# Performance work log

Hardware: AMD Instinct MI355X
Metric: run time of the kernel (lower is better)

The kernel has to match this reference:

```python
import jax, jax.numpy as jnp
import numpy as np

jax.config.update("jax_enable_x64", True)  # original casts scores to float64

D_MODEL = 1024
NUM_HEADS = 16
DEPTH = D_MODEL // NUM_HEADS
B = 2
SQK = 1025  # q/k seq len; scores sliced [1:, :-1] -> 1024
SV = 1024   # v / mask seq len


def _split_heads(x, batch):
    # (B, S, D) -> (B, H, S, depth)
    s = x.shape[1]
    return x.reshape(batch, s, NUM_HEADS, DEPTH).transpose(0, 2, 1, 3)


def setup_inputs() -> dict:
    key = jax.random.key(0)
    ks = jax.random.split(key, 12)
    sc = 1.0 / np.sqrt(D_MODEL)
    inp = {
        "v": jax.random.normal(ks[0], (B, SV, D_MODEL), dtype=jnp.float32),
        "k": jax.random.normal(ks[1], (B, SQK, D_MODEL), dtype=jnp.float32),
        "q": jax.random.normal(ks[2], (B, SQK, D_MODEL), dtype=jnp.float32),
        "mask": jax.random.randint(ks[3], (B, SV, SV), 0, 2, dtype=jnp.int32),
        "Wq0": jax.random.normal(ks[4], (D_MODEL, D_MODEL), dtype=jnp.float32) * sc,
        "bq0": jnp.zeros((D_MODEL,), dtype=jnp.float32),
        "Wk0": jax.random.normal(ks[5], (D_MODEL, D_MODEL), dtype=jnp.float32) * sc,
        "bk0": jnp.zeros((D_MODEL,), dtype=jnp.float32),
        "Wv": jax.random.normal(ks[6], (D_MODEL, D_MODEL), dtype=jnp.float32) * sc,
        "bv": jnp.zeros((D_MODEL,), dtype=jnp.float32),
        "Wo": jax.random.normal(ks[7], (D_MODEL, D_MODEL), dtype=jnp.float32) * sc,
        "bo": jnp.zeros((D_MODEL,), dtype=jnp.float32),
    }
    return inp


def reference(v, k, q, mask, Wq0, bq0, Wk0, bk0, Wv, bv, Wo, bo):
    batch = q.shape[0]
    # projections (wq/wk of the original layer are unused in call)
    qq = q @ Wq0 + bq0                      # (B, SQK, D)
    kk = k @ Wk0 + bk0                      # (B, SQK, D)
    vv = v @ Wv + bv                        # (B, SV, D)
    qh = _split_heads(qq, batch)            # (B, H, SQK, depth)
    kh = _split_heads(kk, batch)
    vh = _split_heads(vv, batch)            # (B, H, SV, depth)

    # custom attention: matmul -> slice -> relu/scale -> fp64 -> mask -> softmax
    scores = jnp.einsum("bhqd,bhkd->bhqk", qh, kh)          # (B,H,SQK,SQK)
    scores = scores[:, :, 1:, :-1]                           # (B,H,SV,SV)
    dk = jnp.float64(DEPTH)
    nl = jax.nn.relu(scores / jnp.sqrt(dk)).astype(jnp.float64)
    nl = nl + mask[:, None, :, :].astype(jnp.float64) * (-1e9)
    att_weights = jax.nn.softmax(nl, axis=-1)                # (B,H,SV,SV) fp64

    out = jnp.einsum("bhqk,bhkd->bhqd", att_weights, vh.astype(jnp.float64))
    out = out.transpose(0, 2, 1, 3).reshape(batch, SV, D_MODEL)  # concat heads
    output = out @ Wo.astype(jnp.float64) + bo.astype(jnp.float64)
    return output, att_weights
```

## Files before the change

### kernel.cpp

```cpp
#include <hip/hip_runtime.h>

#define DM   1024
#define NH   16
#define DH   64
#define BATCH 2
#define SEQ  1024

typedef __attribute__((ext_vector_type(8))) short   short8;
typedef __attribute__((ext_vector_type(4))) float   f32x4;
typedef __attribute__((ext_vector_type(4))) unsigned short ushort4v;

__device__ __forceinline__ unsigned short f2bf(float f) {
  unsigned int u = __float_as_uint(f);
  u += 0x7FFFu + ((u >> 16) & 1u);
  return (unsigned short)(u >> 16);
}
__device__ __forceinline__ float bf2f(unsigned short h) {
  return __uint_as_float(((unsigned int)h) << 16);
}

__device__ __forceinline__ void mfma_gemm(
    const float* __restrict__ A, long lda,
    const unsigned short* __restrict__ BTh,
    const unsigned short* __restrict__ BTl, long ldb,
    const float* __restrict__ bias, float* __restrict__ C, long ldc,
    int K, int row0, int col0)
{
  __shared__ short Ah[4][64][8];
  __shared__ short Al[4][64][8];
  __shared__ short Bh[8][64][8];
  __shared__ short Bl[8][64][8];

  const int tid  = threadIdx.x;
  const int wave = tid >> 6, lane = tid & 63;
  const int wm = wave & 1, wn = wave >> 1;

  f32x4 acc[2][4];
#pragma unroll
  for (int i = 0; i < 2; i++)
#pragma unroll
    for (int j = 0; j < 4; j++) acc[i][j] = (f32x4){0.f, 0.f, 0.f, 0.f};

  const int am    = tid >> 2;
  const int ako   = (tid & 3) * 8;
  const int afrag = am >> 4;
  const int alane = (am & 15) + (ako >> 3) * 16;
  const int bn     = tid >> 1;
  const int bkh    = tid & 1;
  const int bfrag  = bn >> 4;
  const int blane0 = (bn & 15) + (bkh * 2) * 16;

  const float*          aptr  = A   + (long)(row0 + am) * lda + ako;
  const unsigned short* bhptr = BTh + (long)(col0 + bn) * ldb + bkh * 16;
  const unsigned short* blptr = BTl + (long)(col0 + bn) * ldb + bkh * 16;

  for (int k0 = 0; k0 < K; k0 += 32) {
    float4 v0 = *(const float4*)(aptr + k0);
    float4 v1 = *(const float4*)(aptr + k0 + 4);
    float f[8] = {v0.x, v0.y, v0.z, v0.w, v1.x, v1.y, v1.z, v1.w};
    short8 hv, lv;
#pragma unroll
    for (int i = 0; i < 8; i++) {
      unsigned short h = f2bf(f[i]);
      hv[i] = (short)h;
      lv[i] = (short)f2bf(f[i] - bf2f(h));
    }
    *(short8*)&Ah[afrag][alane][0] = hv;
    *(short8*)&Al[afrag][alane][0] = lv;
    short8 b0 = *(const short8*)(bhptr + k0);
    short8 b1 = *(const short8*)(bhptr + k0 + 8);
    short8 c0 = *(const short8*)(blptr + k0);
    short8 c1 = *(const short8*)(blptr + k0 + 8);
    *(short8*)&Bh[bfrag][blane0][0]      = b0;
    *(short8*)&Bh[bfrag][blane0 + 16][0] = b1;
    *(short8*)&Bl[bfrag][blane0][0]      = c0;
    *(short8*)&Bl[bfrag][blane0 + 16][0] = c1;
    __syncthreads();

    short8 a_h[2], a_l[2], b_h[4], b_l[4];
#pragma unroll
    for (int fm = 0; fm < 2; fm++) {
      a_h[fm] = *(short8*)&Ah[wm * 2 + fm][lane][0];
      a_l[fm] = *(short8*)&Al[wm * 2 + fm][lane][0];
    }
#pragma unroll
    for (int fn = 0; fn < 4; fn++) {
      b_h[fn] = *(short8*)&Bh[wn * 4 + fn][lane][0];
      b_l[fn] = *(short8*)&Bl[wn * 4 + fn][lane][0];
    }
#pragma unroll
    for (int fm = 0; fm < 2; fm++)
#pragma unroll
      for (int fn = 0; fn < 4; fn++) {
        acc[fm][fn] = __builtin_amdgcn_mfma_f32_16x16x32_bf16(
            a_h[fm], b_h[fn], acc[fm][fn], 0, 0, 0);
        acc[fm][fn] = __builtin_amdgcn_mfma_f32_16x16x32_bf16(
            a_h[fm], b_l[fn], acc[fm][fn], 0, 0, 0);
        acc[fm][fn] = __builtin_amdgcn_mfma_f32_16x16x32_bf16(
            a_l[fm], b_h[fn], acc[fm][fn], 0, 0, 0);
      }
    __syncthreads();
  }

  const int erow = (lane >> 4) * 4;
  const int ecol = lane & 15;
#pragma unroll
  for (int fm = 0; fm < 2; fm++)
#pragma unroll
    for (int fn = 0; fn < 4; fn++) {
      const int r0 = row0 + wm * 32 + fm * 16 + erow;
      const int cc = col0 + wn * 64 + fn * 16 + ecol;
      const float b = bias ? bias[cc] : 0.f;
#pragma unroll
      for (int i = 0; i < 4; i++)
        C[(long)(r0 + i) * ldc + cc] = acc[fm][fn][i] + b;
    }
}

struct SplitTArgs {
  const float* W[4];
  unsigned short* TH[4];
  unsigned short* TL[4];
};

__global__ __launch_bounds__(256) void splitT_kernel(SplitTArgs s) {
  const int w = blockIdx.z;
  const float* W = s.W[w];
  unsigned short* TH = s.TH[w];
  unsigned short* TL = s.TL[w];
  __shared__ float tile[32][33];
  const int t = threadIdx.x;
  const int k0 = blockIdx.y * 32, n0 = blockIdx.x * 32;
  {
    const int r = t >> 3, c = (t & 7) * 4;
    float4 v = *(const float4*)(W + (long)(k0 + r) * DM + n0 + c);
    tile[r][c] = v.x; tile[r][c + 1] = v.y;
    tile[r][c + 2] = v.z; tile[r][c + 3] = v.w;
  }
  __syncthreads();
  const int n = t >> 3, k = (t & 7) * 4;
  ushort4v h, l;
#pragma unroll
  for (int i = 0; i < 4; i++) {
    float f = tile[k + i][n];
    unsigned short hh = f2bf(f);
    h[i] = hh;
    l[i] = f2bf(f - bf2f(hh));
  }
  *(ushort4v*)(TH + (long)(n0 + n) * DM + k0 + k) = h;
  *(ushort4v*)(TL + (long)(n0 + n) * DM + k0 + k) = l;
}

struct MfmaProjArgs {
  const float* A[3];
  long astride[3];
  const unsigned short* BTh[3];
  const unsigned short* BTl[3];
  const float* bias[3];
  float* C[3];
};

__global__ __launch_bounds__(256) void proj_mfma_kernel(MfmaProjArgs p) {
  const int z = blockIdx.z, sel = z >> 1, b = z & 1;
  const float* A = p.A[sel] + (long)b * p.astride[sel];
  float* C = p.C[sel] + (long)b * SEQ * DM;
  mfma_gemm(A, DM, p.BTh[sel], p.BTl[sel], DM, p.bias[sel], C, DM, DM,
            blockIdx.y * 64, blockIdx.x * 128);
}

__global__ __launch_bounds__(256) void out_mfma_kernel(
    const float* __restrict__ ohs,
    const unsigned short* __restrict__ WoTh,
    const unsigned short* __restrict__ WoTl,
    const float* __restrict__ bo, float* __restrict__ out0) {
  const int b = blockIdx.z;
  mfma_gemm(ohs + (long)b * SEQ * DM, DM, WoTh, WoTl, DM, bo,
            out0 + (long)b * SEQ * DM, DM, DM,
            blockIdx.y * 64, blockIdx.x * 128);
}

__device__ __forceinline__ float score_ep(float a, int m) {
  float s = fmaxf(a * 0.125f, 0.f);
  return m ? (s - 1e9f) : s;
}

__global__ __launch_bounds__(256) void scores_kernel(
    const float* __restrict__ qq, const float* __restrict__ kk,
    const int* __restrict__ mask, float* __restrict__ attw)
{
  const int z = blockIdx.z;
  const int b = z >> 4, h = z & 15;
  const float* Aq = qq + (long)b * (SEQ * DM) + h * DH;
  const float* Bk = kk + (long)b * (SEQ * DM) + h * DH;
  const int*   mk = mask + (long)b * (SEQ * SEQ);
  float* out = attw + (long)z * (SEQ * SEQ);

  constexpr int BM = 128, BK = 16, TM = 8, TN = 8;
  __shared__ float Qs[BK][BM];
  __shared__ float Ks[BK][BM];
  const int tid = threadIdx.x, tx = tid & 15, ty = tid >> 4;
  const int row0 = blockIdx.y * BM, col0 = blockIdx.x * BM;

  float acc[TM][TN];
#pragma unroll
  for (int i = 0; i < TM; i++)
#pragma unroll
    for (int j = 0; j < TN; j++) acc[i][j] = 0.f;

  const int ar = tid >> 1;
  const int ac = (tid & 1) * 8;

  for (int k0 = 0; k0 < DH; k0 += BK) {
    {
      const float* ap = Aq + (long)(row0 + ar) * DM + k0 + ac;
      float4 v0 = *(const float4*)ap;
      float4 v1 = *(const float4*)(ap + 4);
      Qs[ac + 0][ar] = v0.x; Qs[ac + 1][ar] = v0.y;
      Qs[ac + 2][ar] = v0.z; Qs[ac + 3][ar] = v0.w;
      Qs[ac + 4][ar] = v1.x; Qs[ac + 5][ar] = v1.y;
      Qs[ac + 6][ar] = v1.z; Qs[ac + 7][ar] = v1.w;
    }
    {
      const float* bp = Bk + (long)(col0 + ar) * DM + k0 + ac;
      float4 v0 = *(const float4*)bp;
      float4 v1 = *(const float4*)(bp + 4);
      Ks[ac + 0][ar] = v0.x; Ks[ac + 1][ar] = v0.y;
      Ks[ac + 2][ar] = v0.z; Ks[ac + 3][ar] = v0.w;
      Ks[ac + 4][ar] = v1.x; Ks[ac + 5][ar] = v1.y;
      Ks[ac + 6][ar] = v1.z; Ks[ac + 7][ar] = v1.w;
    }
    __syncthreads();
#pragma unroll
    for (int kk2 = 0; kk2 < BK; kk2++) {
      float a[TM], w[TN];
#pragma unroll
      for (int i = 0; i < TM; i++) a[i] = Qs[kk2][ty * TM + i];
#pragma unroll
      for (int j = 0; j < TN; j++) w[j] = Ks[kk2][tx * TN + j];
#pragma unroll
      for (int i = 0; i < TM; i++)
#pragma unroll
        for (int j = 0; j < TN; j++)
          acc[i][j] = fmaf(a[i], w[j], acc[i][j]);
    }
    __syncthreads();
  }

#pragma unroll
  for (int i = 0; i < TM; i++) {
    const int r = row0 + ty * TM + i;
    const int c = col0 + tx * TN;
    const int4* mp = (const int4*)(mk + (long)r * SEQ + c);
    int4 m0 = mp[0], m1 = mp[1];
    float4 v0, v1;
    v0.x = score_ep(acc[i][0], m0.x); v0.y = score_ep(acc[i][1], m0.y);
    v0.z = score_ep(acc[i][2], m0.z); v0.w = score_ep(acc[i][3], m0.w);
    v1.x = score_ep(acc[i][4], m1.x); v1.y = score_ep(acc[i][5], m1.y);
    v1.z = score_ep(acc[i][6], m1.z); v1.w = score_ep(acc[i][7], m1.w);
    float* op = out + (long)r * SEQ + c;
    *(float4*)op       = v0;
    *(float4*)(op + 4) = v1;
  }
}

__global__ __launch_bounds__(256) void softmax_kernel(float* __restrict__ attw)
{
  const long g = blockIdx.x;
  float* row = attw + g * SEQ;
  const int tid = threadIdx.x;
  float4 v = *(float4*)(row + tid * 4);

  float m = fmaxf(fmaxf(v.x, v.y), fmaxf(v.z, v.w));
#pragma unroll
  for (int o = 32; o >= 1; o >>= 1) m = fmaxf(m, __shfl_xor(m, o, 64));
  __shared__ float redm[4];
  const int wave = tid >> 6, lane = tid & 63;
  if (lane == 0) redm[wave] = m;
  __syncthreads();
  m = fmaxf(fmaxf(redm[0], redm[1]), fmaxf(redm[2], redm[3]));

  v.x = __expf(v.x - m); v.y = __expf(v.y - m);
  v.z = __expf(v.z - m); v.w = __expf(v.w - m);
  float s = v.x + v.y + v.z + v.w;
#pragma unroll
  for (int o = 32; o >= 1; o >>= 1) s += __shfl_xor(s, o, 64);
  __shared__ float reds[4];
  if (lane == 0) reds[wave] = s;
  __syncthreads();
  s = reds[0] + reds[1] + reds[2] + reds[3];

  const float inv = 1.0f / s;
  v.x *= inv; v.y *= inv; v.z *= inv; v.w *= inv;
  *(float4*)(row + tid * 4) = v;
}

template<int BN, int TN>
__device__ __forceinline__ void gemm_body(
    const float* __restrict__ A, int lda,
    const float* __restrict__ W, int ldw,
    const float* __restrict__ bias,
    float* __restrict__ C, int ldc, int K)
{
  constexpr int BM = 128, BK = 16, TM = 8;
  __shared__ float As[BK][BM];
  __shared__ float Ws[BK][BN];

  const int tid = threadIdx.x;
  const int tx  = tid & 15;
  const int ty  = tid >> 4;
  const int row0 = blockIdx.y * BM;
  const int col0 = blockIdx.x * BN;

  float acc[TM][TN];
#pragma unroll
  for (int i = 0; i < TM; i++)
#pragma unroll
    for (int j = 0; j < TN; j++) acc[i][j] = 0.f;

  const int ar = tid >> 1;
  const int ac = (tid & 1) * 8;

  for (int k0 = 0; k0 < K; k0 += BK) {
    {
      const float* ap = A + (long)(row0 + ar) * lda + (k0 + ac);
      float4 v0 = *(const float4*)ap;
      float4 v1 = *(const float4*)(ap + 4);
      As[ac + 0][ar] = v0.x; As[ac + 1][ar] = v0.y;
      As[ac + 2][ar] = v0.z; As[ac + 3][ar] = v0.w;
      As[ac + 4][ar] = v1.x; As[ac + 5][ar] = v1.y;
      As[ac + 6][ar] = v1.z; As[ac + 7][ar] = v1.w;
    }
    {
      constexpr int PER = BK * BN / 256;
      const int wr = (tid * PER) / BN;
      const int wc = (tid * PER) % BN;
      const float* wp = W + (long)(k0 + wr) * ldw + col0 + wc;
      if constexpr (PER == 8) {
        *(float4*)&Ws[wr][wc]     = *(const float4*)wp;
        *(float4*)&Ws[wr][wc + 4] = *(const float4*)(wp + 4);
      } else {
        *(float4*)&Ws[wr][wc]     = *(const float4*)wp;
      }
    }
    __syncthreads();
#pragma unroll
    for (int kk = 0; kk < BK; kk++) {
      float a[TM], w[TN];
#pragma unroll
      for (int i = 0; i < TM; i++) a[i] = As[kk][ty * TM + i];
#pragma unroll
      for (int j = 0; j < TN; j++) w[j] = Ws[kk][tx * TN + j];
#pragma unroll
      for (int i = 0; i < TM; i++)
#pragma unroll
        for (int j = 0; j < TN; j++)
          acc[i][j] = fmaf(a[i], w[j], acc[i][j]);
    }
    __syncthreads();
  }

#pragma unroll
  for (int i = 0; i < TM; i++) {
    const int r = row0 + ty * TM + i;
    float* cp = C + (long)r * ldc + col0 + tx * TN;
#pragma unroll
    for (int j = 0; j < TN; j += 4) {
      float4 v;
      v.x = acc[i][j + 0]; v.y = acc[i][j + 1];
      v.z = acc[i][j + 2]; v.w = acc[i][j + 3];
      if (bias) {
        const float* bp = bias + col0 + tx * TN + j;
        v.x += bp[0]; v.y += bp[1]; v.z += bp[2]; v.w += bp[3];
      }
      *(float4*)(cp + j) = v;
    }
  }
}

__global__ __launch_bounds__(256) void pv_kernel(
    const float* __restrict__ attw, const float* __restrict__ vv,
    float* __restrict__ out_hs)
{
  const int z = blockIdx.z, b = z >> 4, h = z & 15;
  gemm_body<64, 4>(attw + (long)z * (SEQ * SEQ), SEQ,
                   vv + (long)b * (SEQ * DM) + h * DH, DM,
                   nullptr,
                   out_hs + (long)b * (SEQ * DM) + h * DH, DM, SEQ);
}

extern "C" void kernel_launch(void* const* d_in, const int* in_sizes, int n_in,
                              void* d_out, int out_size, void* d_ws, size_t ws_size,
                              hipStream_t stream)
{
  const float* v    = (const float*)d_in[0];
  const float* k    = (const float*)d_in[1];
  const float* q    = (const float*)d_in[2];
  const int*   mask = (const int*)  d_in[3];
  const float* Wq   = (const float*)d_in[4];
  const float* bq   = (const float*)d_in[5];
  const float* Wk   = (const float*)d_in[6];
  const float* bk   = (const float*)d_in[7];
  const float* Wv   = (const float*)d_in[8];
  const float* bv   = (const float*)d_in[9];
  const float* Wo   = (const float*)d_in[10];
  const float* bo   = (const float*)d_in[11];

  const long NE = (long)SEQ * DM;
  float* qq  = (float*)d_ws;
  float* kkp = qq  + BATCH * NE;
  float* vvp = kkp + BATCH * NE;
  float* ohs = vvp + BATCH * NE;
  unsigned short* WoTh = (unsigned short*)(ohs + BATCH * NE);
  unsigned short* WoTl = WoTh + NE;

  float* out0 = (float*)d_out;
  float* attw = out0 + BATCH * NE;

  unsigned short* stash = (unsigned short*)(attw + (long)BATCH * NH * SEQ * SEQ)
                          - 6L * NE;
  unsigned short* WqTh = stash;
  unsigned short* WqTl = WqTh + NE;
  unsigned short* WkTh = WqTl + NE;
  unsigned short* WkTl = WkTh + NE;
  unsigned short* WvTh = WkTl + NE;
  unsigned short* WvTl = WvTh + NE;

  dim3 blk(256);

  SplitTArgs st;
  st.W[0] = Wq; st.W[1] = Wk; st.W[2] = Wv; st.W[3] = Wo;
  st.TH[0] = WqTh; st.TH[1] = WkTh; st.TH[2] = WvTh; st.TH[3] = WoTh;
  st.TL[0] = WqTl; st.TL[1] = WkTl; st.TL[2] = WvTl; st.TL[3] = WoTl;
  hipLaunchKernelGGL(splitT_kernel, dim3(32, 32, 4), blk, 0, stream, st);

  MfmaProjArgs p;
  p.A[0] = q + DM;  p.A[1] = k;   p.A[2] = v;
  p.astride[0] = 1025L * DM; p.astride[1] = 1025L * DM; p.astride[2] = 1024L * DM;
  p.BTh[0] = WqTh; p.BTh[1] = WkTh; p.BTh[2] = WvTh;
  p.BTl[0] = WqTl; p.BTl[1] = WkTl; p.BTl[2] = WvTl;
  p.bias[0] = bq;  p.bias[1] = bk;  p.bias[2] = bv;
  p.C[0] = qq;     p.C[1] = kkp;    p.C[2] = vvp;
  hipLaunchKernelGGL(proj_mfma_kernel, dim3(8, 16, 6), blk, 0, stream, p);

  hipLaunchKernelGGL(scores_kernel, dim3(8, 8, 32), blk, 0, stream, qq, kkp, mask, attw);
  hipLaunchKernelGGL(softmax_kernel, dim3(BATCH * NH * SEQ), blk, 0, stream, attw);
  hipLaunchKernelGGL(pv_kernel, dim3(1, 8, 32), blk, 0, stream, attw, vvp, ohs);
  hipLaunchKernelGGL(out_mfma_kernel, dim3(8, 16, 2), blk, 0, stream, ohs, WoTh, WoTl, bo, out0);
}
```

Baseline: 454.8 us.

## Fuse scores, softmax and PV into one two-pass MFMA attention kernel

```diff
diff --git a/kernel.cpp b/kernel.cpp
--- a/kernel.cpp
+++ b/kernel.cpp
@@ -5,6 +5,8 @@
 #define DH   64
 #define BATCH 2
 #define SEQ  1024
+#define QBLK 128
+#define KBLK 128
 
 typedef __attribute__((ext_vector_type(8))) short   short8;
 typedef __attribute__((ext_vector_type(4))) float   f32x4;
@@ -17,6 +19,16 @@
 }
 __device__ __forceinline__ float bf2f(unsigned short h) {
   return __uint_as_float(((unsigned int)h) << 16);
+}
+__device__ __forceinline__ void split8(const float4& a, const float4& b,
+                                       short8& h, short8& l) {
+  float f[8] = {a.x, a.y, a.z, a.w, b.x, b.y, b.z, b.w};
+#pragma unroll
+  for (int j = 0; j < 8; j++) {
+    unsigned short hh = f2bf(f[j]);
+    h[j] = (short)hh;
+    l[j] = (short)f2bf(f[j] - bf2f(hh));
+  }
 }
 
 __device__ __forceinline__ void mfma_gemm(
@@ -57,14 +69,8 @@
   for (int k0 = 0; k0 < K; k0 += 32) {
     float4 v0 = *(const float4*)(aptr + k0);
     float4 v1 = *(const float4*)(aptr + k0 + 4);
-    float f[8] = {v0.x, v0.y, v0.z, v0.w, v1.x, v1.y, v1.z, v1.w};
     short8 hv, lv;
-#pragma unroll
-    for (int i = 0; i < 8; i++) {
-      unsigned short h = f2bf(f[i]);
-      hv[i] = (short)h;
-      lv[i] = (short)f2bf(f[i] - bf2f(h));
-    }
+    split8(v0, v1, hv, lv);
     *(short8*)&Ah[afrag][alane][0] = hv;
     *(short8*)&Al[afrag][alane][0] = lv;
     short8 b0 = *(const short8*)(bhptr + k0);
@@ -179,213 +185,190 @@
             blockIdx.y * 64, blockIdx.x * 128);
 }
 
-__device__ __forceinline__ float score_ep(float a, int m) {
-  float s = fmaxf(a * 0.125f, 0.f);
-  return m ? (s - 1e9f) : s;
-}
-
-__global__ __launch_bounds__(256) void scores_kernel(
+__global__ __launch_bounds__(512) void fused_attn_kernel(
     const float* __restrict__ qq, const float* __restrict__ kk,
-    const int* __restrict__ mask, float* __restrict__ attw)
+    const float* __restrict__ vv, const int* __restrict__ mask,
+    float* __restrict__ attw, float* __restrict__ ohs)
 {
-  const int z = blockIdx.z;
+  const int z = blockIdx.y;
   const int b = z >> 4, h = z & 15;
-  const float* Aq = qq + (long)b * (SEQ * DM) + h * DH;
-  const float* Bk = kk + (long)b * (SEQ * DM) + h * DH;
-  const int*   mk = mask + (long)b * (SEQ * SEQ);
-  float* out = attw + (long)z * (SEQ * SEQ);
-
-  constexpr int BM = 128, BK = 16, TM = 8, TN = 8;
-  __shared__ float Qs[BK][BM];
-  __shared__ float Ks[BK][BM];
-  const int tid = threadIdx.x, tx = tid & 15, ty = tid >> 4;
-  const int row0 = blockIdx.y * BM, col0 = blockIdx.x * BM;
-
-  float acc[TM][TN];
-#pragma unroll
-  for (int i = 0; i < TM; i++)
-#pragma unroll
-    for (int j = 0; j < TN; j++) acc[i][j] = 0.f;
-
-  const int ar = tid >> 1;
-  const int ac = (tid & 1) * 8;
-
-  for (int k0 = 0; k0 < DH; k0 += BK) {
+  const int row0 = blockIdx.x * QBLK;
+
+  const float* Q = qq + (long)b * SEQ * DM + h * DH;
+  const float* K = kk + (long)b * SEQ * DM + h * DH;
+  const float* V = vv + (long)b * SEQ * DM + h * DH;
+  const int*  mk = mask + (long)b * SEQ * SEQ;
+  float* att  = attw + (long)z * SEQ * SEQ;
+  float* ohsb = ohs + (long)b * SEQ * DM + h * DH;
+
+  __shared__ short Kh[8][2][64][8];
+  __shared__ short Kl[8][2][64][8];
+  __shared__ short Vh[4][4][64][8];
+  __shared__ short Vl[4][4][64][8];
+  __shared__ float P[8][16][132];
+
+  const int tid  = threadIdx.x;
+  const int w    = tid >> 6, lane = tid & 63;
+  const int lg   = lane >> 4, lr = lane & 15;
+  const int grow = row0 + 16 * w + 4 * lg;
+
+  short8 qh[2], ql[2];
+  {
+    const float* qp = Q + (long)(row0 + 16 * w + lr) * DM + 8 * lg;
+#pragma unroll
+    for (int kh = 0; kh < 2; kh++) {
+      float4 a = *(const float4*)(qp + 32 * kh);
+      float4 bq = *(const float4*)(qp + 32 * kh + 4);
+      split8(a, bq, qh[kh], ql[kh]);
+    }
+  }
+
+  float lsum[4] = {0.f, 0.f, 0.f, 0.f};
+  for (int t = 0; t < 8; t++) {
     {
-      const float* ap = Aq + (long)(row0 + ar) * DM + k0 + ac;
-      float4 v0 = *(const float4*)ap;
-      float4 v1 = *(const float4*)(ap + 4);
-      Qs[ac + 0][ar] = v0.x; Qs[ac + 1][ar] = v0.y;
-      Qs[ac + 2][ar] = v0.z; Qs[ac + 3][ar] = v0.w;
-      Qs[ac + 4][ar] = v1.x; Qs[ac + 5][ar] = v1.y;
-      Qs[ac + 6][ar] = v1.z; Qs[ac + 7][ar] = v1.w;
-    }
+      const int key = tid >> 2, d0 = (tid & 3) * 16;
+      const float* kp = K + (long)(t * KBLK + key) * DM + d0;
+#pragma unroll
+      for (int oct = 0; oct < 2; oct++) {
+        const int d = d0 + 8 * oct;
+        float4 x = *(const float4*)(kp + 8 * oct);
+        float4 y = *(const float4*)(kp + 8 * oct + 4);
+        short8 hs;
+        float f[8] = {x.x, x.y, x.z, x.w, y.x, y.y, y.z, y.w};
+#pragma unroll
+        for (int j = 0; j < 8; j++) hs[j] = (short)f2bf(f[j]);
+        *(short8*)&Kh[key >> 4][d >> 5][(key & 15) + 16 * ((d & 31) >> 3)][0] = hs;
+      }
+    }
+    __syncthreads();
+
+    f32x4 s[8];
+#pragma unroll
+    for (int nf = 0; nf < 8; nf++) s[nf] = (f32x4){0.f, 0.f, 0.f, 0.f};
+#pragma unroll
+    for (int nf = 0; nf < 8; nf++)
+#pragma unroll
+      for (int kh = 0; kh < 2; kh++) {
+        short8 kf = *(short8*)&Kh[nf][kh][lane][0];
+        s[nf] = __builtin_amdgcn_mfma_f32_16x16x32_bf16(qh[kh], kf, s[nf], 0, 0, 0);
+      }
+#pragma unroll
+    for (int nf = 0; nf < 8; nf++)
+#pragma unroll
+      for (int i = 0; i < 4; i++) {
+        int m = mk[(long)(grow + i) * SEQ + t * KBLK + 16 * nf + lr];
+        float se = fmaxf(s[nf][i] * 0.125f, 0.f) - 1e9f * (float)m;
+        lsum[i] += __expf(se);
+      }
+    __syncthreads();
+  }
+#pragma unroll
+  for (int o = 1; o <= 8; o <<= 1)
+#pragma unroll
+    for (int i = 0; i < 4; i++)
+      lsum[i] += __shfl_xor(lsum[i], o, 64);
+  float linv[4];
+#pragma unroll
+  for (int i = 0; i < 4; i++) linv[i] = 1.f / lsum[i];
+
+  f32x4 o_acc[4];
+#pragma unroll
+  for (int nf = 0; nf < 4; nf++) o_acc[nf] = (f32x4){0.f, 0.f, 0.f, 0.f};
+
+  for (int t = 0; t < 8; t++) {
     {
-      const float* bp = Bk + (long)(col0 + ar) * DM + k0 + ac;
-      float4 v0 = *(const float4*)bp;
-      float4 v1 = *(const float4*)(bp + 4);
-      Ks[ac + 0][ar] = v0.x; Ks[ac + 1][ar] = v0.y;
-      Ks[ac + 2][ar] = v0.z; Ks[ac + 3][ar] = v0.w;
-      Ks[ac + 4][ar] = v1.x; Ks[ac + 5][ar] = v1.y;
-      Ks[ac + 6][ar] = v1.z; Ks[ac + 7][ar] = v1.w;
-    }
-    __syncthreads();
-#pragma unroll
-    for (int kk2 = 0; kk2 < BK; kk2++) {
-      float a[TM], w[TN];
-#pragma unroll
-      for (int i = 0; i < TM; i++) a[i] = Qs[kk2][ty * TM + i];
-#pragma unroll
-      for (int j = 0; j < TN; j++) w[j] = Ks[kk2][tx * TN + j];
-#pragma unroll
-      for (int i = 0; i < TM; i++)
-#pragma unroll
-        for (int j = 0; j < TN; j++)
-          acc[i][j] = fmaf(a[i], w[j], acc[i][j]);
-    }
-    __syncthreads();
-  }
-
-#pragma unroll
-  for (int i = 0; i < TM; i++) {
-    const int r = row0 + ty * TM + i;
-    const int c = col0 + tx * TN;
-    const int4* mp = (const int4*)(mk + (long)r * SEQ + c);
-    int4 m0 = mp[0], m1 = mp[1];
-    float4 v0, v1;
-    v0.x = score_ep(acc[i][0], m0.x); v0.y = score_ep(acc[i][1], m0.y);
-    v0.z = score_ep(acc[i][2], m0.z); v0.w = score_ep(acc[i][3], m0.w);
-    v1.x = score_ep(acc[i][4], m1.x); v1.y = score_ep(acc[i][5], m1.y);
-    v1.z = score_ep(acc[i][6], m1.z); v1.w = score_ep(acc[i][7], m1.w);
-    float* op = out + (long)r * SEQ + c;
-    *(float4*)op       = v0;
-    *(float4*)(op + 4) = v1;
-  }
-}
-
-__global__ __launch_bounds__(256) void softmax_kernel(float* __restrict__ attw)
-{
-  const long g = blockIdx.x;
-  float* row = attw + g * SEQ;
-  const int tid = threadIdx.x;
-  float4 v = *(float4*)(row + tid * 4);
-
-  float m = fmaxf(fmaxf(v.x, v.y), fmaxf(v.z, v.w));
-#pragma unroll
-  for (int o = 32; o >= 1; o >>= 1) m = fmaxf(m, __shfl_xor(m, o, 64));
-  __shared__ float redm[4];
-  const int wave = tid >> 6, lane = tid & 63;
-  if (lane == 0) redm[wave] = m;
-  __syncthreads();
-  m = fmaxf(fmaxf(redm[0], redm[1]), fmaxf(redm[2], redm[3]));
-
-  v.x = __expf(v.x - m); v.y = __expf(v.y - m);
-  v.z = __expf(v.z - m); v.w = __expf(v.w - m);
-  float s = v.x + v.y + v.z + v.w;
-#pragma unroll
-  for (int o = 32; o >= 1; o >>= 1) s += __shfl_xor(s, o, 64);
-  __shared__ float reds[4];
-  if (lane == 0) reds[wave] = s;
-  __syncthreads();
-  s = reds[0] + reds[1] + reds[2] + reds[3];
-
-  const float inv = 1.0f / s;
-  v.x *= inv; v.y *= inv; v.z *= inv; v.w *= inv;
-  *(float4*)(row + tid * 4) = v;
-}
-
-template<int BN, int TN>
-__device__ __forceinline__ void gemm_body(
-    const float* __restrict__ A, int lda,
-    const float* __restrict__ W, int ldw,
-    const float* __restrict__ bias,
-    float* __restrict__ C, int ldc, int K)
-{
-  constexpr int BM = 128, BK = 16, TM = 8;
-  __shared__ float As[BK][BM];
-  __shared__ float Ws[BK][BN];
-
-  const int tid = threadIdx.x;
-  const int tx  = tid & 15;
-  const int ty  = tid >> 4;
-  const int row0 = blockIdx.y * BM;
-  const int col0 = blockIdx.x * BN;
-
-  float acc[TM][TN];
-#pragma unroll
-  for (int i = 0; i < TM; i++)
-#pragma unroll
-    for (int j = 0; j < TN; j++) acc[i][j] = 0.f;
-
-  const int ar = tid >> 1;
-  const int ac = (tid & 1) * 8;
-
-  for (int k0 = 0; k0 < K; k0 += BK) {
-    {
-      const float* ap = A + (long)(row0 + ar) * lda + (k0 + ac);
-      float4 v0 = *(const float4*)ap;
-      float4 v1 = *(const float4*)(ap + 4);
-      As[ac + 0][ar] = v0.x; As[ac + 1][ar] = v0.y;
-      As[ac + 2][ar] = v0.z; As[ac + 3][ar] = v0.w;
-      As[ac + 4][ar] = v1.x; As[ac + 5][ar] = v1.y;
-      As[ac + 6][ar] = v1.z; As[ac + 7][ar] = v1.w;
-    }
-    {
-      constexpr int PER = BK * BN / 256;
-      const int wr = (tid * PER) / BN;
-      const int wc = (tid * PER) % BN;
-      const float* wp = W + (long)(k0 + wr) * ldw + col0 + wc;
-      if constexpr (PER == 8) {
-        *(float4*)&Ws[wr][wc]     = *(const float4*)wp;
-        *(float4*)&Ws[wr][wc + 4] = *(const float4*)(wp + 4);
-      } else {
-        *(float4*)&Ws[wr][wc]     = *(const float4*)wp;
-      }
-    }
-    __syncthreads();
-#pragma unroll
-    for (int kk = 0; kk < BK; kk++) {
-      float a[TM], w[TN];
-#pragma unroll
-      for (int i = 0; i < TM; i++) a[i] = As[kk][ty * TM + i];
-#pragma unroll
-      for (int j = 0; j < TN; j++) w[j] = Ws[kk][tx * TN + j];
-#pragma unroll
-      for (int i = 0; i < TM; i++)
-#pragma unroll
-        for (int j = 0; j < TN; j++)
-          acc[i][j] = fmaf(a[i], w[j], acc[i][j]);
-    }
-    __syncthreads();
-  }
-
-#pragma unroll
-  for (int i = 0; i < TM; i++) {
-    const int r = row0 + ty * TM + i;
-    float* cp = C + (long)r * ldc + col0 + tx * TN;
-#pragma unroll
-    for (int j = 0; j < TN; j += 4) {
-      float4 v;
-      v.x = acc[i][j + 0]; v.y = acc[i][j + 1];
-      v.z = acc[i][j + 2]; v.w = acc[i][j + 3];
-      if (bias) {
-        const float* bp = bias + col0 + tx * TN + j;
-        v.x += bp[0]; v.y += bp[1]; v.z += bp[2]; v.w += bp[3];
-      }
-      *(float4*)(cp + j) = v;
-    }
-  }
-}
-
-__global__ __launch_bounds__(256) void pv_kernel(
-    const float* __restrict__ attw, const float* __restrict__ vv,
-    float* __restrict__ out_hs)
-{
-  const int z = blockIdx.z, b = z >> 4, h = z & 15;
-  gemm_body<64, 4>(attw + (long)z * (SEQ * SEQ), SEQ,
-                   vv + (long)b * (SEQ * DM) + h * DH, DM,
-                   nullptr,
-                   out_hs + (long)b * (SEQ * DM) + h * DH, DM, SEQ);
+      const int key = tid >> 2, d0 = (tid & 3) * 16;
+      const float* kp = K + (long)(t * KBLK + key) * DM + d0;
+#pragma unroll
+      for (int oct = 0; oct < 2; oct++) {
+        const int d = d0 + 8 * oct;
+        float4 x = *(const float4*)(kp + 8 * oct);
+        float4 y = *(const float4*)(kp + 8 * oct + 4);
+        short8 hs, ls;
+        split8(x, y, hs, ls);
+        const int nf2 = key >> 4, kh2 = d >> 5;
+        const int ln2 = (key & 15) + 16 * ((d & 31) >> 3);
+        *(short8*)&Kh[nf2][kh2][ln2][0] = hs;
+        *(short8*)&Kl[nf2][kh2][ln2][0] = ls;
+      }
+    }
+#pragma unroll
+    for (int r = 0; r < 4; r++) {
+      const int idx = tid + 512 * r;
+      const int key = idx >> 4, d0 = (idx & 15) * 4;
+      float4 x = *(const float4*)(V + (long)(t * KBLK + key) * DM + d0);
+      const int ks = key >> 5, kin = key & 31;
+      const int g2 = kin >> 3, j2 = kin & 7;
+      float f[4] = {x.x, x.y, x.z, x.w};
+#pragma unroll
+      for (int i = 0; i < 4; i++) {
+        const int d = d0 + i;
+        unsigned short hh = f2bf(f[i]);
+        Vh[ks][d >> 4][(d & 15) + 16 * g2][j2] = (short)hh;
+        Vl[ks][d >> 4][(d & 15) + 16 * g2][j2] = (short)f2bf(f[i] - bf2f(hh));
+      }
+    }
+    __syncthreads();
+
+    f32x4 s[8];
+#pragma unroll
+    for (int nf = 0; nf < 8; nf++) s[nf] = (f32x4){0.f, 0.f, 0.f, 0.f};
+#pragma unroll
+    for (int nf = 0; nf < 8; nf++)
+#pragma unroll
+      for (int kh = 0; kh < 2; kh++) {
+        short8 kfh = *(short8*)&Kh[nf][kh][lane][0];
+        short8 kfl = *(short8*)&Kl[nf][kh][lane][0];
+        s[nf] = __builtin_amdgcn_mfma_f32_16x16x32_bf16(qh[kh], kfh, s[nf], 0, 0, 0);
+        s[nf] = __builtin_amdgcn_mfma_f32_16x16x32_bf16(qh[kh], kfl, s[nf], 0, 0, 0);
+        s[nf] = __builtin_amdgcn_mfma_f32_16x16x32_bf16(ql[kh], kfh, s[nf], 0, 0, 0);
+      }
+
+#pragma unroll
+    for (int nf = 0; nf < 8; nf++)
+#pragma unroll
+      for (int i = 0; i < 4; i++) {
+        int m = mk[(long)(grow + i) * SEQ + t * KBLK + 16 * nf + lr];
+        float se = fmaxf(s[nf][i] * 0.125f, 0.f) - 1e9f * (float)m;
+        P[w][4 * lg + i][16 * nf + lr] = __expf(se) * linv[i];
+      }
+
+    short8 pah[4], pal[4];
+#pragma unroll
+    for (int ks = 0; ks < 4; ks++) {
+      float4 x = *(float4*)&P[w][lr][32 * ks + 8 * lg];
+      float4 y = *(float4*)&P[w][lr][32 * ks + 8 * lg + 4];
+      split8(x, y, pah[ks], pal[ks]);
+    }
+
+#pragma unroll
+    for (int ks = 0; ks < 4; ks++)
+#pragma unroll
+      for (int nf = 0; nf < 4; nf++) {
+        short8 vfh = *(short8*)&Vh[ks][nf][lane][0];
+        short8 vfl = *(short8*)&Vl[ks][nf][lane][0];
+        o_acc[nf] = __builtin_amdgcn_mfma_f32_16x16x32_bf16(pah[ks], vfh, o_acc[nf], 0, 0, 0);
+        o_acc[nf] = __builtin_amdgcn_mfma_f32_16x16x32_bf16(pah[ks], vfl, o_acc[nf], 0, 0, 0);
+        o_acc[nf] = __builtin_amdgcn_mfma_f32_16x16x32_bf16(pal[ks], vfh, o_acc[nf], 0, 0, 0);
+      }
+
+#pragma unroll
+    for (int rh = 0; rh < 2; rh++)
+#pragma unroll
+      for (int rr = 0; rr < 4; rr++) {
+        const int rl = 8 * rh + (lane >> 3);
+        const int c4 = (lane & 7) + 8 * rr;
+        float4 pv4 = *(float4*)&P[w][rl][4 * c4];
+        *(float4*)(att + (long)(row0 + 16 * w + rl) * SEQ + t * KBLK + 4 * c4) = pv4;
+      }
+    __syncthreads();
+  }
+
+#pragma unroll
+  for (int nf = 0; nf < 4; nf++)
+#pragma unroll
+    for (int i = 0; i < 4; i++)
+      ohsb[(long)(grow + i) * DM + 16 * nf + lr] = o_acc[nf][i];
 }
 
 extern "C" void kernel_launch(void* const* d_in, const int* in_sizes, int n_in,
@@ -442,8 +425,9 @@
   p.C[0] = qq;     p.C[1] = kkp;    p.C[2] = vvp;
   hipLaunchKernelGGL(proj_mfma_kernel, dim3(8, 16, 6), blk, 0, stream, p);
 
-  hipLaunchKernelGGL(scores_kernel, dim3(8, 8, 32), blk, 0, stream, qq, kkp, mask, attw);
-  hipLaunchKernelGGL(softmax_kernel, dim3(BATCH * NH * SEQ), blk, 0, stream, attw);
-  hipLaunchKernelGGL(pv_kernel, dim3(1, 8, 32), blk, 0, stream, attw, vvp, ohs);
-  hipLaunchKernelGGL(out_mfma_kernel, dim3(8, 16, 2), blk, 0, stream, ohs, WoTh, WoTl, bo, out0);
-}
+  hipLaunchKernelGGL(fused_attn_kernel, dim3(SEQ / QBLK, BATCH * NH),
+                     dim3(512), 0, stream, qq, kkp, vvp, mask, attw, ohs);
+
+  hipLaunchKernelGGL(out_mfma_kernel, dim3(8, 16, 2), blk, 0, stream,
+                     ohs, WoTh, WoTl, bo, out0);
+}
```

Result: faster. 385.8 us (-15.2%).
